# Kernel optimization log

Hardware: AMD Instinct MI355X
Metric: run time of the kernel (lower is better)

## Reference

```python
import jax, jax.numpy as jnp
import numpy as np

N = 100000   # nodes
E = 1000000  # edges
F_IN = 64    # in_ch
HID = 64     # hid_ch
CLS = 32     # num_classes


def _linear_params(key, out_dim, in_dim):
    kw, kb = jax.random.split(key)
    w = jax.random.normal(kw, (out_dim, in_dim), dtype=jnp.float32) * 0.05
    b = jax.random.normal(kb, (out_dim,), dtype=jnp.float32) * 0.05
    return w, b


def setup_inputs() -> dict:
    key = jax.random.key(0)
    ks = jax.random.split(key, 9)
    x = jax.random.normal(ks[0], (N, F_IN), dtype=jnp.float32)
    edge_index = jax.random.randint(ks[1], (2, E), 0, N, dtype=jnp.int64)
    # conv1: pre Linear(2F->F), post Linear(4F->HID), lin Linear(HID->HID)
    W1_pre, b1_pre = _linear_params(ks[2], F_IN, 2 * F_IN)
    W1_post, b1_post = _linear_params(ks[3], HID, 4 * F_IN)
    W1_lin, b1_lin = _linear_params(ks[4], HID, HID)
    # conv2: pre Linear(2H->H), post Linear(4H->HID), lin Linear(HID->HID)
    W2_pre, b2_pre = _linear_params(ks[5], HID, 2 * HID)
    W2_post, b2_post = _linear_params(ks[6], HID, 4 * HID)
    W2_lin, b2_lin = _linear_params(ks[7], HID, HID)
    # final classifier Linear(HID->CLS)
    Wf, bf = _linear_params(ks[8], CLS, HID)
    return {
        "x": x, "edge_index": edge_index,
        "W1_pre": W1_pre, "b1_pre": b1_pre, "W1_post": W1_post, "b1_post": b1_post,
        "W1_lin": W1_lin, "b1_lin": b1_lin,
        "W2_pre": W2_pre, "b2_pre": b2_pre, "W2_post": W2_post, "b2_post": b2_post,
        "W2_lin": W2_lin, "b2_lin": b2_lin,
        "Wf": Wf, "bf": bf,
    }


def _pna_conv(x, src, dst, Wpre, bpre, Wpost, bpost, Wlin, blin):
    """PyG PNAConv (towers=1, pre/post_layers=1, scalers=['identity'])."""
    n = x.shape[0]
    # message: pre_nn(cat([x_i, x_j]))  (i = target = dst, j = source = src)
    h = jnp.concatenate([x[dst], x[src]], axis=-1)  # [E, 2F]
    m = h @ Wpre.T + bpre                            # [E, F]
    # multi-aggregation at target nodes: mean, max, sum
    s = jax.ops.segment_sum(m, dst, num_segments=n)                    # [N, F]
    cnt = jax.ops.segment_sum(jnp.ones((m.shape[0],), m.dtype), dst,
                              num_segments=n)                          # [N]
    mean = s / jnp.maximum(cnt, 1.0)[:, None]
    mx = jax.ops.segment_max(m, dst, num_segments=n)
    mx = jnp.where(jnp.isfinite(mx), mx, jnp.zeros_like(mx))  # empty -> 0 (PyG)
    agg = jnp.concatenate([mean, mx, s], axis=-1)              # [N, 3F]
    out = jnp.concatenate([x, agg], axis=-1) @ Wpost.T + bpost # [N, HID]
    return out @ Wlin.T + blin


def reference(x, edge_index, W1_pre, b1_pre, W1_post, b1_post, W1_lin, b1_lin,
              W2_pre, b2_pre, W2_post, b2_post, W2_lin, b2_lin, Wf, bf):
    src = edge_index[0]
    dst = edge_index[1]
    h = jax.nn.relu(_pna_conv(x, src, dst, W1_pre, b1_pre, W1_post, b1_post,
                              W1_lin, b1_lin))
    h = jax.nn.relu(_pna_conv(h, src, dst, W2_pre, b2_pre, W2_post, b2_post,
                              W2_lin, b2_lin))
    return h @ Wf.T + bf  # [N, CLS]
```

## Files before the change

### kernel.cpp

```cpp
#include <hip/hip_runtime.h>

#define NN 100000
#define NE 1000000
#define NCLS 32
#define NB 391
#define GN 32
#define NGROUPS (NN/GN)
#define UVG ((NN+63)/64)

typedef __bf16 bf16x8 __attribute__((ext_vector_type(8)));
typedef float f32x16 __attribute__((ext_vector_type(16)));

__device__ __forceinline__ unsigned pk_hi(unsigned u1, unsigned u0){
  return __builtin_amdgcn_perm(u1, u0, 0x07060302u);
}
__device__ __forceinline__ unsigned pk_lo(float f0, float f1, unsigned u0, unsigned u1){
  float r0 = f0 - __uint_as_float(u0 & 0xFFFF0000u);
  float r1 = f1 - __uint_as_float(u1 & 0xFFFF0000u);
  return pk_hi(__float_as_uint(r1), __float_as_uint(r0));
}
__device__ __forceinline__ f32x16 mfma_b(uint4 a, uint4 b, f32x16 c){
  bf16x8 av, bv;
  __builtin_memcpy(&av, &a, 16);
  __builtin_memcpy(&bv, &b, 16);
  return __builtin_amdgcn_mfma_f32_32x32x16_bf16(av, bv, c, 0, 0, 0);
}
__device__ __forceinline__ int crow(int r, int half){ return (r&3) + 8*(r>>2) + 4*half; }

__global__ void k_setup(const float* __restrict__ W1_lin, const float* __restrict__ b1_lin,
                        const float* __restrict__ W1_post, const float* __restrict__ b1_post,
                        const float* __restrict__ W2_lin, const float* __restrict__ b2_lin,
                        const float* __restrict__ W2_post, const float* __restrict__ b2_post,
                        const float* __restrict__ W1_pre, const float* __restrict__ W2_pre,
                        const float* __restrict__ Wf,
                        uint4* __restrict__ Wcf, uint4* __restrict__ Wpf,
                        uint4* __restrict__ Wff, float* __restrict__ bc,
                        int* __restrict__ deg){
  const int blk = blockIdx.x, tid = threadIdx.x;
  if (blk < 16){
    int i = blk*256 + tid;
    int layer = i >> 11;
    int t = (i >> 10) & 1, step = (i >> 6) & 15, lane = i & 63;
    const float* Wlin  = layer ? W2_lin  : W1_lin;
    const float* Wpost = layer ? W2_post : W1_post;
    int col = t*32 + (lane & 31);
    int k0 = step*16 + ((lane >> 5) << 3);
    unsigned hi[4], lo[4];
    for (int p = 0; p < 4; p++){
      float f0 = 0.f, f1 = 0.f;
      for (int j = 0; j < 64; j++){
        float wl = Wlin[col*64 + j];
        f0 += wl * Wpost[j*256 + k0 + 2*p];
        f1 += wl * Wpost[j*256 + k0 + 2*p + 1];
      }
      unsigned u0 = __float_as_uint(f0), u1 = __float_as_uint(f1);
      hi[p] = pk_hi(u1, u0);
      lo[p] = pk_lo(f0, f1, u0, u1);
    }
    uint4* base = Wcf + layer*4096;
    base[t*1024     + step*64 + lane] = make_uint4(hi[0],hi[1],hi[2],hi[3]);
    base[(2+t)*1024 + step*64 + lane] = make_uint4(lo[0],lo[1],lo[2],lo[3]);
  } else if (blk < 24){
    int i = (blk-16)*256 + tid;
    int layer = i >> 10;
    int t = (i >> 8) & 3, st = (i >> 6) & 3, lane = i & 63;
    const float* Wpre = layer ? W2_pre : W1_pre;
    int col = t*32 + (lane & 31);
    int o = col & 63, koff = (col >> 6) * 64;
    int k0 = st*16 + ((lane >> 5) << 3);
    unsigned hi[4], lo[4];
    for (int p = 0; p < 4; p++){
      float f0 = Wpre[o*128 + koff + k0 + 2*p];
      float f1 = Wpre[o*128 + koff + k0 + 2*p + 1];
      unsigned u0 = __float_as_uint(f0), u1 = __float_as_uint(f1);
      hi[p] = pk_hi(u1, u0);
      lo[p] = pk_lo(f0, f1, u0, u1);
    }
    uint4* base = Wpf + layer*2048 + t*512;
    base[st*64 + lane]       = make_uint4(hi[0],hi[1],hi[2],hi[3]);
    base[256 + st*64 + lane] = make_uint4(lo[0],lo[1],lo[2],lo[3]);
  } else if (blk == 24){
    int st = tid >> 6, lane = tid & 63;
    int cls = lane & 31;
    int k0 = st*16 + ((lane >> 5) << 3);
    unsigned hi[4], lo[4];
    for (int p = 0; p < 4; p++){
      float f0 = Wf[cls*64 + k0 + 2*p];
      float f1 = Wf[cls*64 + k0 + 2*p + 1];
      unsigned u0 = __float_as_uint(f0), u1 = __float_as_uint(f1);
      hi[p] = pk_hi(u1, u0);
      lo[p] = pk_lo(f0, f1, u0, u1);
    }
    Wff[st*64 + lane]       = make_uint4(hi[0],hi[1],hi[2],hi[3]);
    Wff[256 + st*64 + lane] = make_uint4(lo[0],lo[1],lo[2],lo[3]);
  } else if (blk == 25){
    if (tid < 128){
      int layer = tid >> 6, o = tid & 63;
      const float* Wlin  = layer ? W2_lin  : W1_lin;
      const float* blin  = layer ? b2_lin  : b1_lin;
      const float* bpost = layer ? b2_post : b1_post;
      float s = blin[o];
      for (int j = 0; j < 64; j++) s += Wlin[o*64+j] * bpost[j];
      bc[tid] = s;
    }
  } else {
    int i = (blk-26)*256 + tid;
    if (i < NN) deg[i] = 0;
  }
}

__global__ void k_deg(const int* __restrict__ dst, int* __restrict__ deg){
  int e = blockIdx.x*256 + threadIdx.x;
  if (e < NE) atomicAdd(&deg[dst[e]], 1);
}

__global__ void k_scan1(const int* __restrict__ deg, int* __restrict__ inc,
                        int* __restrict__ part){
  __shared__ int s[256];
  int tid = threadIdx.x;
  int i = blockIdx.x*256 + tid;
  s[tid] = (i < NN) ? deg[i] : 0;
  __syncthreads();
  for (int off = 1; off < 256; off <<= 1){
    int t = (tid >= off) ? s[tid-off] : 0;
    __syncthreads();
    s[tid] += t;
    __syncthreads();
  }
  inc[i] = s[tid];
  if (tid == 255) part[blockIdx.x] = s[255];
}

__global__ void k_scan23(const int* __restrict__ inc, const int* __restrict__ part,
                         const int* __restrict__ deg,
                         int* __restrict__ rowptr, int* __restrict__ cursor){
  __shared__ int s[512];
  int tid = threadIdx.x;
  s[tid] = (tid < NB) ? part[tid] : 0;
  __syncthreads();
  for (int off = 1; off < 512; off <<= 1){
    int t = (tid >= off) ? s[tid-off] : 0;
    __syncthreads();
    s[tid] += t;
    __syncthreads();
  }
  int b = blockIdx.x;
  int base = b ? s[b-1] : 0;
  if (tid < 256){
    int i = b*256 + tid;
    if (i < NN){
      int inclusive = inc[i] + base;
      rowptr[i+1] = inclusive;
      cursor[i] = inclusive - deg[i];
    }
  }
  if (b == 0 && tid == 0) rowptr[0] = 0;
}

__global__ void k_scatter(const int* __restrict__ src, const int* __restrict__ dst,
                          int* __restrict__ cursor, int* __restrict__ srcs){
  int e = blockIdx.x*256 + threadIdx.x;
  if (e < NE){
    int d = dst[e];
    int p = atomicAdd(&cursor[d], 1);
    srcs[p] = src[e];
  }
}

__global__ __launch_bounds__(512, 4) void k_uv(
    const float* __restrict__ xin, const uint4* __restrict__ Wpf,
    const float* __restrict__ bpre, float* __restrict__ u, float* __restrict__ v){
  __shared__ __align__(16) unsigned XH[64*36];
  __shared__ __align__(16) unsigned XL[64*36];
  const int tid = threadIdx.x;
  const int lane = tid & 63;
  const int w = tid >> 6;
  const int t = w >> 1, rg = w & 1;
  const int cc = lane & 31, half = lane >> 5;
  const int col = t*32 + cc;
  uint4 wfr[2][4];
  {
    const uint4* p = Wpf + t*512;
    #pragma unroll
    for (int s = 0; s < 2; s++)
      #pragma unroll
      for (int st = 0; st < 4; st++) wfr[s][st] = p[s*256 + st*64 + lane];
  }
  const float bias = (t < 2) ? bpre[col] : 0.f;
  float* const dstp = (t < 2) ? u : v;
  const int dcol = col & 63;
  const int srow = tid >> 3, sq = tid & 7;

  for (int g = blockIdx.x; g < UVG; g += gridDim.x){
    const int n0 = g*64;
    __syncthreads();
    {
      const int node = n0 + srow;
      float4 a = {0,0,0,0}, b = {0,0,0,0};
      if (node < NN){
        a = *(const float4*)&xin[(size_t)node*64 + sq*8];
        b = *(const float4*)&xin[(size_t)node*64 + sq*8 + 4];
      }
      unsigned ax = __float_as_uint(a.x), ay = __float_as_uint(a.y);
      unsigned az = __float_as_uint(a.z), aw = __float_as_uint(a.w);
      unsigned bx = __float_as_uint(b.x), by = __float_as_uint(b.y);
      unsigned bz = __float_as_uint(b.z), bw = __float_as_uint(b.w);
      uint4 hi, lo;
      hi.x = pk_hi(ay, ax); lo.x = pk_lo(a.x, a.y, ax, ay);
      hi.y = pk_hi(aw, az); lo.y = pk_lo(a.z, a.w, az, aw);
      hi.z = pk_hi(by, bx); lo.z = pk_lo(b.x, b.y, bx, by);
      hi.w = pk_hi(bw, bz); lo.w = pk_lo(b.z, b.w, bz, bw);
      *(uint4*)&XH[srow*36 + sq*4] = hi;
      *(uint4*)&XL[srow*36 + sq*4] = lo;
    }
    __syncthreads();
    f32x16 acc = {};
    const int arow = (rg*32 + cc)*36 + half*4;
    #pragma unroll
    for (int st = 0; st < 4; st++){
      uint4 ah = *(const uint4*)&XH[arow + st*8];
      uint4 al = *(const uint4*)&XL[arow + st*8];
      acc = mfma_b(ah, wfr[0][st], acc);
      acc = mfma_b(al, wfr[0][st], acc);
      acc = mfma_b(ah, wfr[1][st], acc);
    }
    #pragma unroll
    for (int r = 0; r < 16; r++){
      int row = n0 + rg*32 + crow(r, half);
      if (row < NN) dstp[(size_t)row*64 + dcol] = acc[r] + bias;
    }
  }
}

template<int EPI>
__global__ __launch_bounds__(512, 8) void k_agg(
    const float* __restrict__ xin, const float* __restrict__ u,
    const float* __restrict__ v,
    const int* __restrict__ rowptr, const int* __restrict__ srcs,
    const uint4* __restrict__ Wcf, const float* __restrict__ bcv,
    const uint4* __restrict__ Wff, const float* __restrict__ bfv,
    float* __restrict__ hout, float* __restrict__ outp){
  __shared__ __align__(16) unsigned Zh[GN*132];
  __shared__ __align__(16) unsigned Zl[GN*132];
  const int tid = threadIdx.x;
  const int lane = tid & 63;
  const int w = tid >> 6;
  const int c = lane & 31;
  const int h = lane >> 5;
  const float bias = (w < 2) ? bcv[w*32 + c] : 0.f;
  const uint4* WH = Wcf + w*1024;
  const uint4* WL = Wcf + (2+w)*1024;

  for (int g = blockIdx.x; g < NGROUPS; g += gridDim.x){
    const int n0 = g*GN;
    __syncthreads();
    for (int nn = 0; nn < 4; nn++){
      const int node = n0 + w*4 + nn;
      const int r0 = rowptr[node], r1 = rowptr[node+1];
      const float2 up = *(const float2*)&u[(size_t)node*64 + 2*c];
      const float2 xv = *(const float2*)&xin[(size_t)node*64 + 2*c];
      float Sx = 0.f, Sy = 0.f;
      float Mx = -3.402823466e+38f, My = Mx;
      int j = r0 + h;
      for (; j + 6 < r1; j += 8){
        int s0 = srcs[j], s1 = srcs[j+2], s2 = srcs[j+4], s3 = srcs[j+6];
        float2 a0 = *(const float2*)&v[(size_t)s0*64 + 2*c];
        float2 a1 = *(const float2*)&v[(size_t)s1*64 + 2*c];
        float2 a2 = *(const float2*)&v[(size_t)s2*64 + 2*c];
        float2 a3 = *(const float2*)&v[(size_t)s3*64 + 2*c];
        Sx += (a0.x + a1.x) + (a2.x + a3.x);
        Sy += (a0.y + a1.y) + (a2.y + a3.y);
        Mx = fmaxf(Mx, fmaxf(fmaxf(a0.x, a1.x), fmaxf(a2.x, a3.x)));
        My = fmaxf(My, fmaxf(fmaxf(a0.y, a1.y), fmaxf(a2.y, a3.y)));
      }
      for (; j < r1; j += 2){
        float2 a = *(const float2*)&v[(size_t)srcs[j]*64 + 2*c];
        Sx += a.x; Sy += a.y;
        Mx = fmaxf(Mx, a.x); My = fmaxf(My, a.y);
      }
      Sx += __shfl_xor(Sx, 32, 64);
      Sy += __shfl_xor(Sy, 32, 64);
      Mx = fmaxf(Mx, __shfl_xor(Mx, 32, 64));
      My = fmaxf(My, __shfl_xor(My, 32, 64));

      const int d = r1 - r0;
      float2 z1, z2, z3;
      if (d > 0){
        float fd = (float)d;
        z1.x = up.x + Sx/fd;  z1.y = up.y + Sy/fd;
        z2.x = up.x + Mx;     z2.y = up.y + My;
        z3.x = fmaf(fd, up.x, Sx); z3.y = fmaf(fd, up.y, Sy);
      } else {
        z1.x=z1.y=z2.x=z2.y=z3.x=z3.y=0.f;
      }
      const int row = w*4 + nn;
      float2 q[4] = {xv, z1, z2, z3};
      #pragma unroll
      for (int qq = 0; qq < 4; qq++){
        unsigned u0 = __float_as_uint(q[qq].x), u1 = __float_as_uint(q[qq].y);
        if (h == 0) Zh[row*132 + qq*32 + c] = pk_hi(u1, u0);
        else        Zl[row*132 + qq*32 + c] = pk_lo(q[qq].x, q[qq].y, u0, u1);
      }
    }
    __syncthreads();
    f32x16 acc = {};
    if (w < 2){
      const int arow = c*132 + h*4;
      #pragma unroll 4
      for (int s = 0; s < 16; s++){
        uint4 ah = *(const uint4*)&Zh[arow + s*8];
        uint4 al = *(const uint4*)&Zl[arow + s*8];
        uint4 bh = WH[s*64 + lane];
        uint4 bl = WL[s*64 + lane];
        acc = mfma_b(ah, bh, acc);
        acc = mfma_b(al, bh, acc);
        acc = mfma_b(ah, bl, acc);
      }
      if (EPI == 0){
        #pragma unroll
        for (int r = 0; r < 16; r++){
          float val = fmaxf(acc[r] + bias, 0.f);
          hout[(size_t)(n0 + crow(r,h))*64 + w*32 + c] = val;
        }
      }
    }
    if (EPI == 1){
      __syncthreads();
      if (w < 2){
        float* HF = (float*)Zh;
        #pragma unroll
        for (int r = 0; r < 16; r++){
          float val = fmaxf(acc[r] + bias, 0.f);
          HF[crow(r,h)*64 + w*32 + c] = val;
        }
      }
      __syncthreads();
      {
        const float* HF = (const float*)Zh;
        unsigned* HH = Zl;
        unsigned* HL = Zl + 1152;
        const int row = tid >> 4, p4 = tid & 15;
        float4 f = *(const float4*)&HF[row*64 + p4*4];
        unsigned f0 = __float_as_uint(f.x), f1 = __float_as_uint(f.y);
        unsigned f2 = __float_as_uint(f.z), f3 = __float_as_uint(f.w);
        HH[row*36 + p4*2]   = pk_hi(f1, f0);
        HH[row*36 + p4*2+1] = pk_hi(f3, f2);
        HL[row*36 + p4*2]   = pk_lo(f.x, f.y, f0, f1);
        HL[row*36 + p4*2+1] = pk_lo(f.z, f.w, f2, f3);
      }
      __syncthreads();
      if (w == 0){
        f32x16 ac2 = {};
        const unsigned* HH = Zl;
        const unsigned* HL = Zl + 1152;
        const int arow = c*36 + h*4;
        #pragma unroll
        for (int st = 0; st < 4; st++){
          uint4 ah = *(const uint4*)&HH[arow + st*8];
          uint4 al = *(const uint4*)&HL[arow + st*8];
          uint4 bh = Wff[st*64 + lane];
          uint4 bl = Wff[256 + st*64 + lane];
          ac2 = mfma_b(ah, bh, ac2);
          ac2 = mfma_b(al, bh, ac2);
          ac2 = mfma_b(ah, bl, ac2);
        }
        const float bcls = bfv[c];
        #pragma unroll
        for (int r = 0; r < 16; r++)
          outp[(size_t)(n0 + crow(r,h))*NCLS + c] = ac2[r] + bcls;
      }
    }
  }
}

extern "C" void kernel_launch(void* const* d_in, const int* in_sizes, int n_in,
                              void* d_out, int out_size, void* d_ws, size_t ws_size,
                              hipStream_t stream){
  const float* x      = (const float*)d_in[0];
  const int*   ei     = (const int*)  d_in[1];
  const int*   src    = ei;
  const int*   dst    = ei + NE;
  const float* W1_pre = (const float*)d_in[2];
  const float* b1_pre = (const float*)d_in[3];
  const float* W1_post= (const float*)d_in[4];
  const float* b1_post= (const float*)d_in[5];
  const float* W1_lin = (const float*)d_in[6];
  const float* b1_lin = (const float*)d_in[7];
  const float* W2_pre = (const float*)d_in[8];
  const float* b2_pre = (const float*)d_in[9];
  const float* W2_post= (const float*)d_in[10];
  const float* b2_post= (const float*)d_in[11];
  const float* W2_lin = (const float*)d_in[12];
  const float* b2_lin = (const float*)d_in[13];
  const float* Wf     = (const float*)d_in[14];
  const float* bf     = (const float*)d_in[15];
  float* out = (float*)d_out;

  size_t off = 0;
  char* ws = (char*)d_ws;
  auto alloc = [&](size_t bytes){ void* p = ws + off; off += (bytes + 255) & ~(size_t)255; return p; };
  int*   deg    = (int*)  alloc(NN*4);
  int*   rowptr = (int*)  alloc((NN+1)*4);
  int*   cursor = (int*)  alloc(NN*4);
  int*   inc    = (int*)  alloc(NB*256*4);
  int*   part   = (int*)  alloc(512*4);
  int*   srcs   = (int*)  alloc((size_t)NE*4);
  float* u      = (float*)alloc((size_t)NN*64*4);
  float* v      = (float*)alloc((size_t)NN*64*4);
  float* h1     = (float*)alloc((size_t)NN*64*4);
  uint4* Wcf    = (uint4*)alloc(2*4096*16);
  uint4* Wpf    = (uint4*)alloc(4096*16);
  uint4* Wff    = (uint4*)alloc(512*16);
  float* bc     = (float*)alloc(128*4);

  k_setup<<<417, 256, 0, stream>>>(W1_lin, b1_lin, W1_post, b1_post,
                                   W2_lin, b2_lin, W2_post, b2_post,
                                   W1_pre, W2_pre, Wf, Wcf, Wpf, Wff, bc, deg);
  k_deg    <<<(NE+255)/256, 256, 0, stream>>>(dst, deg);
  k_scan1  <<<NB, 256, 0, stream>>>(deg, inc, part);
  k_scan23 <<<NB, 512, 0, stream>>>(inc, part, deg, rowptr, cursor);
  k_scatter<<<(NE+255)/256, 256, 0, stream>>>(src, dst, cursor, srcs);

  k_uv    <<<1024, 512, 0, stream>>>(x, Wpf, b1_pre, u, v);
  k_agg<0><<<1024, 512, 0, stream>>>(x, u, v, rowptr, srcs, Wcf, bc,
                                     nullptr, nullptr, h1, nullptr);

  k_uv    <<<1024, 512, 0, stream>>>(h1, Wpf + 2048, b2_pre, u, v);
  k_agg<1><<<1024, 512, 0, stream>>>(h1, u, v, rowptr, srcs, Wcf + 4096, bc + 64,
                                     Wff, bf, nullptr, out);
}
```

Baseline: 331.6 us.

## Store gathered message table in bf16 and software-pipeline neighbor index loads

k_uv now writes the source-side projection v as packed bf16 pairs instead of fp32, halving the bytes gathered per edge in k_agg. The aggregation loop processes two nodes per pass and prefetches the next batch of neighbor indices before issuing the current gathers, aiming to hide the index-load latency. The k_agg grid doubles from 1024 to 2048 blocks. This trades precision on the per-edge messages, since sum and max now run over bf16-rounded values, for lower gather bandwidth.

```diff
diff --git a/kernel.cpp b/kernel.cpp
--- a/kernel.cpp
+++ b/kernel.cpp
@@ -169,7 +169,7 @@
 
 __global__ __launch_bounds__(512, 4) void k_uv(
     const float* __restrict__ xin, const uint4* __restrict__ Wpf,
-    const float* __restrict__ bpre, float* __restrict__ u, float* __restrict__ v){
+    const float* __restrict__ bpre, float* __restrict__ u, unsigned* __restrict__ vq){
   __shared__ __align__(16) unsigned XH[64*36];
   __shared__ __align__(16) unsigned XL[64*36];
   const int tid = threadIdx.x;
@@ -187,7 +187,6 @@
       for (int st = 0; st < 4; st++) wfr[s][st] = p[s*256 + st*64 + lane];
   }
   const float bias = (t < 2) ? bpre[col] : 0.f;
-  float* const dstp = (t < 2) ? u : v;
   const int dcol = col & 63;
   const int srow = tid >> 3, sq = tid & 7;
 
@@ -224,10 +223,24 @@
       acc = mfma_b(al, wfr[0][st], acc);
       acc = mfma_b(ah, wfr[1][st], acc);
     }
-    #pragma unroll
-    for (int r = 0; r < 16; r++){
-      int row = n0 + rg*32 + crow(r, half);
-      if (row < NN) dstp[(size_t)row*64 + dcol] = acc[r] + bias;
+    if (t < 2){
+      #pragma unroll
+      for (int r = 0; r < 16; r++){
+        int row = n0 + rg*32 + crow(r, half);
+        if (row < NN) u[(size_t)row*64 + dcol] = acc[r] + bias;
+      }
+    } else {
+      #pragma unroll
+      for (int r = 0; r < 16; r++){
+        float val = acc[r];
+        float pv = __shfl_xor(val, 1, 64);
+        if ((cc & 1) == 0){
+          unsigned pk;
+          asm("v_cvt_pk_bf16_f32 %0, %1, %2" : "=v"(pk) : "v"(val), "v"(pv));
+          int row = n0 + rg*32 + crow(r, half);
+          if (row < NN) vq[(size_t)row*32 + (dcol >> 1)] = pk;
+        }
+      }
     }
   }
 }
@@ -235,7 +248,7 @@
 template<int EPI>
 __global__ __launch_bounds__(512, 8) void k_agg(
     const float* __restrict__ xin, const float* __restrict__ u,
-    const float* __restrict__ v,
+    const unsigned* __restrict__ vq,
     const int* __restrict__ rowptr, const int* __restrict__ srcs,
     const uint4* __restrict__ Wcf, const float* __restrict__ bcv,
     const uint4* __restrict__ Wff, const float* __restrict__ bfv,
@@ -254,52 +267,75 @@
   for (int g = blockIdx.x; g < NGROUPS; g += gridDim.x){
     const int n0 = g*GN;
     __syncthreads();
-    for (int nn = 0; nn < 4; nn++){
-      const int node = n0 + w*4 + nn;
-      const int r0 = rowptr[node], r1 = rowptr[node+1];
-      const float2 up = *(const float2*)&u[(size_t)node*64 + 2*c];
-      const float2 xv = *(const float2*)&xin[(size_t)node*64 + 2*c];
-      float Sx = 0.f, Sy = 0.f;
-      float Mx = -3.402823466e+38f, My = Mx;
-      int j = r0 + h;
-      for (; j + 6 < r1; j += 8){
-        int s0 = srcs[j], s1 = srcs[j+2], s2 = srcs[j+4], s3 = srcs[j+6];
-        float2 a0 = *(const float2*)&v[(size_t)s0*64 + 2*c];
-        float2 a1 = *(const float2*)&v[(size_t)s1*64 + 2*c];
-        float2 a2 = *(const float2*)&v[(size_t)s2*64 + 2*c];
-        float2 a3 = *(const float2*)&v[(size_t)s3*64 + 2*c];
-        Sx += (a0.x + a1.x) + (a2.x + a3.x);
-        Sy += (a0.y + a1.y) + (a2.y + a3.y);
-        Mx = fmaxf(Mx, fmaxf(fmaxf(a0.x, a1.x), fmaxf(a2.x, a3.x)));
-        My = fmaxf(My, fmaxf(fmaxf(a0.y, a1.y), fmaxf(a2.y, a3.y)));
-      }
-      for (; j < r1; j += 2){
-        float2 a = *(const float2*)&v[(size_t)srcs[j]*64 + 2*c];
-        Sx += a.x; Sy += a.y;
-        Mx = fmaxf(Mx, a.x); My = fmaxf(My, a.y);
-      }
-      Sx += __shfl_xor(Sx, 32, 64);
-      Sy += __shfl_xor(Sy, 32, 64);
-      Mx = fmaxf(Mx, __shfl_xor(Mx, 32, 64));
-      My = fmaxf(My, __shfl_xor(My, 32, 64));
-
-      const int d = r1 - r0;
-      float2 z1, z2, z3;
-      if (d > 0){
-        float fd = (float)d;
-        z1.x = up.x + Sx/fd;  z1.y = up.y + Sy/fd;
-        z2.x = up.x + Mx;     z2.y = up.y + My;
-        z3.x = fmaf(fd, up.x, Sx); z3.y = fmaf(fd, up.y, Sy);
-      } else {
-        z1.x=z1.y=z2.x=z2.y=z3.x=z3.y=0.f;
-      }
-      const int row = w*4 + nn;
-      float2 q[4] = {xv, z1, z2, z3};
+    #pragma unroll
+    for (int pr = 0; pr < 2; pr++){
+      const int nA = n0 + w*4 + pr*2;
+      const int r0A = rowptr[nA],   r1A = rowptr[nA+1];
+      const int r0B = rowptr[nA+1], r1B = rowptr[nA+2];
+      int jA = r0A + h, jB = r0B + h;
+      int a0=0,a1=0,a2=0,a3=0, b0=0,b1=0,b2=0,b3=0;
+      bool hA = (jA + 6 < r1A), hB = (jB + 6 < r1B);
+      if (hA){ a0=srcs[jA]; a1=srcs[jA+2]; a2=srcs[jA+4]; a3=srcs[jA+6]; }
+      if (hB){ b0=srcs[jB]; b1=srcs[jB+2]; b2=srcs[jB+4]; b3=srcs[jB+6]; }
       #pragma unroll
-      for (int qq = 0; qq < 4; qq++){
-        unsigned u0 = __float_as_uint(q[qq].x), u1 = __float_as_uint(q[qq].y);
-        if (h == 0) Zh[row*132 + qq*32 + c] = pk_hi(u1, u0);
-        else        Zl[row*132 + qq*32 + c] = pk_lo(q[qq].x, q[qq].y, u0, u1);
+      for (int sub = 0; sub < 2; sub++){
+        const int node = nA + sub;
+        const int r1 = sub ? r1B : r1A;
+        int jj = sub ? jB : jA;
+        int e0 = sub?b0:a0, e1 = sub?b1:a1, e2 = sub?b2:a2, e3 = sub?b3:a3;
+        bool have = sub ? hB : hA;
+        float Sx = 0.f, Sy = 0.f;
+        float Mx = -3.402823466e+38f, My = Mx;
+        while (have){
+          int njj = jj + 8;
+          bool more = (njj + 6 < r1);
+          int f0=0,f1=0,f2=0,f3=0;
+          if (more){ f0=srcs[njj]; f1=srcs[njj+2]; f2=srcs[njj+4]; f3=srcs[njj+6]; }
+          unsigned p0 = vq[(size_t)e0*32 + c];
+          unsigned p1 = vq[(size_t)e1*32 + c];
+          unsigned p2 = vq[(size_t)e2*32 + c];
+          unsigned p3 = vq[(size_t)e3*32 + c];
+          float x0 = __uint_as_float(p0 << 16), y0 = __uint_as_float(p0 & 0xFFFF0000u);
+          float x1 = __uint_as_float(p1 << 16), y1 = __uint_as_float(p1 & 0xFFFF0000u);
+          float x2 = __uint_as_float(p2 << 16), y2 = __uint_as_float(p2 & 0xFFFF0000u);
+          float x3 = __uint_as_float(p3 << 16), y3 = __uint_as_float(p3 & 0xFFFF0000u);
+          Sx += (x0 + x1) + (x2 + x3);
+          Sy += (y0 + y1) + (y2 + y3);
+          Mx = fmaxf(Mx, fmaxf(fmaxf(x0, x1), fmaxf(x2, x3)));
+          My = fmaxf(My, fmaxf(fmaxf(y0, y1), fmaxf(y2, y3)));
+          jj = njj; e0=f0; e1=f1; e2=f2; e3=f3; have = more;
+        }
+        for (; jj < r1; jj += 2){
+          unsigned p = vq[(size_t)srcs[jj]*32 + c];
+          float x0 = __uint_as_float(p << 16), y0 = __uint_as_float(p & 0xFFFF0000u);
+          Sx += x0; Sy += y0;
+          Mx = fmaxf(Mx, x0); My = fmaxf(My, y0);
+        }
+        Sx += __shfl_xor(Sx, 32, 64);
+        Sy += __shfl_xor(Sy, 32, 64);
+        Mx = fmaxf(Mx, __shfl_xor(Mx, 32, 64));
+        My = fmaxf(My, __shfl_xor(My, 32, 64));
+
+        const float2 up = *(const float2*)&u[(size_t)node*64 + 2*c];
+        const float2 xv = *(const float2*)&xin[(size_t)node*64 + 2*c];
+        const int d = r1 - (sub ? r0B : r0A);
+        float2 z1, z2, z3;
+        if (d > 0){
+          float fd = (float)d;
+          z1.x = up.x + Sx/fd;  z1.y = up.y + Sy/fd;
+          z2.x = up.x + Mx;     z2.y = up.y + My;
+          z3.x = fmaf(fd, up.x, Sx); z3.y = fmaf(fd, up.y, Sy);
+        } else {
+          z1.x=z1.y=z2.x=z2.y=z3.x=z3.y=0.f;
+        }
+        const int row = w*4 + pr*2 + sub;
+        float2 q[4] = {xv, z1, z2, z3};
+        #pragma unroll
+        for (int qq = 0; qq < 4; qq++){
+          unsigned u0 = __float_as_uint(q[qq].x), u1 = __float_as_uint(q[qq].y);
+          if (h == 0) Zh[row*132 + qq*32 + c] = pk_hi(u1, u0);
+          else        Zl[row*132 + qq*32 + c] = pk_lo(q[qq].x, q[qq].y, u0, u1);
+        }
       }
     }
     __syncthreads();
@@ -399,19 +435,19 @@
   size_t off = 0;
   char* ws = (char*)d_ws;
   auto alloc = [&](size_t bytes){ void* p = ws + off; off += (bytes + 255) & ~(size_t)255; return p; };
-  int*   deg    = (int*)  alloc(NN*4);
-  int*   rowptr = (int*)  alloc((NN+1)*4);
-  int*   cursor = (int*)  alloc(NN*4);
-  int*   inc    = (int*)  alloc(NB*256*4);
-  int*   part   = (int*)  alloc(512*4);
-  int*   srcs   = (int*)  alloc((size_t)NE*4);
-  float* u      = (float*)alloc((size_t)NN*64*4);
-  float* v      = (float*)alloc((size_t)NN*64*4);
-  float* h1     = (float*)alloc((size_t)NN*64*4);
-  uint4* Wcf    = (uint4*)alloc(2*4096*16);
-  uint4* Wpf    = (uint4*)alloc(4096*16);
-  uint4* Wff    = (uint4*)alloc(512*16);
-  float* bc     = (float*)alloc(128*4);
+  int*      deg    = (int*)     alloc(NN*4);
+  int*      rowptr = (int*)     alloc((NN+1)*4);
+  int*      cursor = (int*)     alloc(NN*4);
+  int*      inc    = (int*)     alloc(NB*256*4);
+  int*      part   = (int*)     alloc(512*4);
+  int*      srcs   = (int*)     alloc((size_t)NE*4);
+  float*    u      = (float*)   alloc((size_t)NN*64*4);
+  unsigned* vq     = (unsigned*)alloc((size_t)NN*32*4);
+  float*    h1     = (float*)   alloc((size_t)NN*64*4);
+  uint4*    Wcf    = (uint4*)   alloc(2*4096*16);
+  uint4*    Wpf    = (uint4*)   alloc(4096*16);
+  uint4*    Wff    = (uint4*)   alloc(512*16);
+  float*    bc     = (float*)   alloc(128*4);
 
   k_setup<<<417, 256, 0, stream>>>(W1_lin, b1_lin, W1_post, b1_post,
                                    W2_lin, b2_lin, W2_post, b2_post,
@@ -421,11 +457,11 @@
   k_scan23 <<<NB, 512, 0, stream>>>(inc, part, deg, rowptr, cursor);
   k_scatter<<<(NE+255)/256, 256, 0, stream>>>(src, dst, cursor, srcs);
 
-  k_uv    <<<1024, 512, 0, stream>>>(x, Wpf, b1_pre, u, v);
-  k_agg<0><<<1024, 512, 0, stream>>>(x, u, v, rowptr, srcs, Wcf, bc,
+  k_uv    <<<1024, 512, 0, stream>>>(x, Wpf, b1_pre, u, vq);
+  k_agg<0><<<2048, 512, 0, stream>>>(x, u, vq, rowptr, srcs, Wcf, bc,
                                      nullptr, nullptr, h1, nullptr);
 
-  k_uv    <<<1024, 512, 0, stream>>>(h1, Wpf + 2048, b2_pre, u, v);
-  k_agg<1><<<1024, 512, 0, stream>>>(h1, u, v, rowptr, srcs, Wcf + 4096, bc + 64,
+  k_uv    <<<1024, 512, 0, stream>>>(h1, Wpf + 2048, b2_pre, u, vq);
+  k_agg<1><<<2048, 512, 0, stream>>>(h1, u, vq, rowptr, srcs, Wcf + 4096, bc + 64,
                                      Wff, bf, nullptr, out);
 }
```

Result: faster. 310.0 us (-6.5%).
